# Kernel tuning notes

Measured on AMD Instinct MI355X. Metric: run time of the kernel, lower is better.

The kernel has to match this reference:

```python
import jax, jax.numpy as jnp
import numpy as np
from jax import lax

NPOINT = 1024
RADIUS = 0.2
NSAMPLE = 32


def fps(xyz, npoint):
    """Furthest point sampling on one cloud. xyz: (N,3) -> (npoint,) int32."""
    n = xyz.shape[0]
    init_d = jnp.full((n,), 1e10, xyz.dtype)

    def body(carry, _):
        dists, last_idx = carry
        last = xyz[last_idx]
        d = jnp.sum((xyz - last) ** 2, axis=-1)
        dists = jnp.minimum(dists, d)
        nxt = jnp.argmax(dists).astype(jnp.int32)
        return (dists, nxt), nxt

    (_, _), idxs = lax.scan(body, (init_d, jnp.int32(0)), None, length=npoint - 1)
    return jnp.concatenate([jnp.zeros((1,), jnp.int32), idxs])


def ball_query(xyz, new_xyz, radius, nsample):
    """First `nsample` points of xyz within `radius` of each center (pad with first hit).
    xyz: (N,3), new_xyz: (S,3) -> (S,nsample) int32."""
    n = xyz.shape[0]
    d2 = jnp.sum((new_xyz[:, None, :] - xyz[None, :, :]) ** 2, axis=-1)  # (S,N)
    cand = jnp.where(d2 < radius * radius, jnp.arange(n, dtype=jnp.int32)[None, :], n)
    idx = jnp.sort(cand, axis=1)[:, :nsample]                            # (S,K)
    first = jnp.where(idx[:, :1] == n, 0, idx[:, :1])
    return jnp.where(idx == n, first, idx)


def setup_inputs() -> dict:
    key = jax.random.key(0)
    ks = jax.random.split(key, 8)
    C_in = 64 + 3  # features + relative xyz
    W1 = jax.random.normal(ks[0], (64, C_in), jnp.float32) * (1.0 / np.sqrt(C_in))
    b1 = jnp.zeros((64,), jnp.float32)
    W2 = jax.random.normal(ks[1], (128, 64), jnp.float32) * (1.0 / np.sqrt(64))
    b2 = jnp.zeros((128,), jnp.float32)
    W3 = jax.random.normal(ks[2], (256, 128), jnp.float32) * (1.0 / np.sqrt(128))
    b3 = jnp.zeros((256,), jnp.float32)
    xyz = jax.random.uniform(ks[3], (8, 4096, 3), jnp.float32)
    features = jax.random.normal(ks[4], (8, 4096, 64), jnp.float32)
    return {"xyz": xyz, "features": features, "W1": W1, "b1": b1,
            "W2": W2, "b2": b2, "W3": W3, "b3": b3}


def reference(xyz, features, W1, b1, W2, b2, W3, b3):
    def per_batch(xyz_b, feat_b):
        fps_idx = fps(xyz_b, NPOINT)                      # (S,)
        new_xyz = xyz_b[fps_idx]                          # (S,3)
        idx = ball_query(xyz_b, new_xyz, RADIUS, NSAMPLE)  # (S,K)
        g_xyz = xyz_b[idx] - new_xyz[:, None, :]          # (S,K,3) relative coords
        g_feat = feat_b[idx]                              # (S,K,C)
        g = jnp.concatenate([g_xyz, g_feat], axis=-1)     # (S,K,3+C)
        x = jnp.transpose(g, (2, 0, 1))                   # (C',S,K)
        for W, b in ((W1, b1), (W2, b2), (W3, b3)):       # 1x1 conv + ReLU stack
            x = jax.nn.relu(jnp.einsum('oc,csk->osk', W, x) + b[:, None, None])
        return new_xyz, jnp.max(x, axis=-1), fps_idx      # max-pool over nsample

    new_xyz, new_features, sample_inds = jax.vmap(per_batch)(xyz, features)
    return new_xyz, new_features, sample_inds
```

## Files before the change

### kernel.cpp

```cpp
#include <hip/hip_runtime.h>
#include <stdint.h>

#define N_PTS 4096
#define S_PTS 1024
#define K_SAMP 32
#define NWORK 248
#define RSTRIDE 16

typedef __attribute__((ext_vector_type(8))) short bf16x8;
typedef __attribute__((ext_vector_type(4))) float f32x4;

#define GT1_S 104
#define GT2_S 72
#define GT3_S 136

__device__ __forceinline__ short f2b(float f){
  unsigned u = __float_as_uint(f);
  u = u + 0x7fffu + ((u >> 16) & 1u);
  return (short)(u >> 16);
}

#define DPP_QUAD_XOR1 0xB1
#define DPP_QUAD_XOR2 0x4E
#define DPP_ROW_HMIRR 0x141
#define DPP_ROW_MIRR  0x140
#define DPP_ROW_BC15  0x142
#define DPP_ROW_BC31  0x143

template<int CTRL>
__device__ __forceinline__ unsigned long long kstep(unsigned long long k){
  unsigned lo = (unsigned)k, hi = (unsigned)(k >> 32);
  unsigned lo2 = (unsigned)__builtin_amdgcn_update_dpp((int)lo, (int)lo, CTRL, 0xF, 0xF, false);
  unsigned hi2 = (unsigned)__builtin_amdgcn_update_dpp((int)hi, (int)hi, CTRL, 0xF, 0xF, false);
  unsigned long long ok = ((unsigned long long)hi2 << 32) | lo2;
  return ok > k ? ok : k;
}

__global__ void wconv_kernel(const float* __restrict__ W1,
                             const float* __restrict__ W2,
                             const float* __restrict__ W3,
                             short* __restrict__ ws_w,
                             int* __restrict__ ready){
  short* w1 = ws_w;
  short* w2 = ws_w + 64*96;
  short* w3 = ws_w + 64*96 + 128*64;
  int t = blockIdx.x * blockDim.x + threadIdx.x;
  int stride = gridDim.x * blockDim.x;
  for (int i = t; i < 8*S_PTS*RSTRIDE; i += stride) ready[i] = 0;
  for (int i = t; i < 64*96; i += stride){
    int m = i / 96, k = i - m*96;
    float v = 0.0f;
    if (k < 64)      v = W1[m*67 + 3 + k];
    else if (k < 67) v = W1[m*67 + (k - 64)];
    w1[i] = f2b(v);
  }
  for (int i = t; i < 128*64;  i += stride) w2[i] = f2b(W2[i]);
  for (int i = t; i < 256*128; i += stride) w3[i] = f2b(W3[i]);
}

template<int M, int KC, int KPAD, int GS_IN, int GS_OUT>
__device__ __forceinline__ void layer_mfma(const short* __restrict__ Wl,
                                           const short* gin, short* gout,
                                           const float* __restrict__ sbias_l,
                                           int w, int quad, int col){
  for (int m0 = w*16; m0 < M; m0 += 64){
    f32x4 acc0 = {0,0,0,0}, acc1 = {0,0,0,0};
#pragma unroll
    for (int kc = 0; kc < KC; ++kc){
      bf16x8 a  = *reinterpret_cast<const bf16x8*>(Wl + (size_t)(m0+col)*KPAD + kc*32 + quad*8);
      bf16x8 b0 = *reinterpret_cast<const bf16x8*>(gin + col*GS_IN + kc*32 + quad*8);
      bf16x8 b1 = *reinterpret_cast<const bf16x8*>(gin + (16+col)*GS_IN + kc*32 + quad*8);
      acc0 = __builtin_amdgcn_mfma_f32_16x16x32_bf16(a, b0, acc0, 0, 0, 0);
      acc1 = __builtin_amdgcn_mfma_f32_16x16x32_bf16(a, b1, acc1, 0, 0, 0);
    }
    int rbase = m0 + quad*4;
    unsigned long long P0 = 0ull, P1 = 0ull;
#pragma unroll
    for (int r = 0; r < 4; ++r){
      float bias = sbias_l[rbase + r];
      unsigned long long q0 = (unsigned short)f2b(fmaxf(acc0[r] + bias, 0.0f));
      unsigned long long q1 = (unsigned short)f2b(fmaxf(acc1[r] + bias, 0.0f));
      P0 |= q0 << (16*r);
      P1 |= q1 << (16*r);
    }
    *reinterpret_cast<unsigned long long*>(&gout[col*GS_OUT + rbase])      = P0;
    *reinterpret_cast<unsigned long long*>(&gout[(16+col)*GS_OUT + rbase]) = P1;
  }
}

__global__ __launch_bounds__(256) void fused_kernel(
    const float* __restrict__ xyz, const float* __restrict__ feat,
    const float* __restrict__ b1, const float* __restrict__ b2,
    const float* __restrict__ b3, const short* __restrict__ ws_w,
    float* __restrict__ out_newxyz, float* __restrict__ out_inds,
    int* __restrict__ ready, float* __restrict__ out_feat){

  __shared__ __align__(16) union ShU {
    struct { float4 c4[N_PTS]; unsigned long long slots[2][4]; } f;
    struct { short gT1[32*GT1_S]; short gT2[32*GT2_S]; short gT3[32*GT3_S];
             int sidx[K_SAMP]; float sbias[448]; int cidx; } m;
    char pad[82400];
  } sh;

  const int t = threadIdx.x;
  const int lane = t & 63;
  const int w = t >> 6;

  if (blockIdx.x < 8){
    const int b = blockIdx.x;
    const float* xb = xyz + (size_t)b * N_PTS * 3;

    float px[16], py[16], pz[16], dist[16];
#pragma unroll
    for (int j = 0; j < 16; ++j){
      int p = j * 256 + t;
      float x = xb[p*3+0], y = xb[p*3+1], z = xb[p*3+2];
      px[j] = x; py[j] = y; pz[j] = z; dist[j] = 1e10f;
      sh.f.c4[p] = make_float4(x, y, z, 0.0f);
    }
    __syncthreads();

    float lx, ly, lz;
    { float4 c0 = sh.f.c4[0]; lx = c0.x; ly = c0.y; lz = c0.z; }
    if (t == 0){
      out_inds[(size_t)b * S_PTS] = 0.0f;
      out_newxyz[(size_t)b*S_PTS*3 + 0] = lx;
      out_newxyz[(size_t)b*S_PTS*3 + 1] = ly;
      out_newxyz[(size_t)b*S_PTS*3 + 2] = lz;
      __hip_atomic_store(&ready[(size_t)b*S_PTS*RSTRIDE], 1,
                         __ATOMIC_RELAXED, __HIP_MEMORY_SCOPE_AGENT);
    }

    for (int it = 1; it < S_PTS; ++it){
      float bv = -1.0f; int bj = 0;
#pragma unroll
      for (int j = 0; j < 16; ++j){
        float dx = __fsub_rn(px[j], lx);
        float dy = __fsub_rn(py[j], ly);
        float dz = __fsub_rn(pz[j], lz);
        float d  = __fadd_rn(__fadd_rn(__fmul_rn(dx,dx), __fmul_rn(dy,dy)), __fmul_rn(dz,dz));
        float nd = fminf(dist[j], d);
        dist[j] = nd;
        bool gt = nd > bv;
        bv = gt ? nd : bv;
        bj = gt ? j  : bj;
      }
      int bi = bj * 256 + t;
      unsigned long long k = ((unsigned long long)__float_as_uint(bv) << 32)
                           | (unsigned)(~bi);

      k = kstep<DPP_QUAD_XOR1>(k);
      k = kstep<DPP_QUAD_XOR2>(k);
      k = kstep<DPP_ROW_HMIRR>(k);
      k = kstep<DPP_ROW_MIRR >(k);
      k = kstep<DPP_ROW_BC15 >(k);
      k = kstep<DPP_ROW_BC31 >(k);

      if (lane == 63) sh.f.slots[it & 1][w] = k;
      __syncthreads();

      unsigned long long sk = sh.f.slots[it & 1][lane & 3];
      sk = kstep<DPP_QUAD_XOR1>(sk);
      sk = kstep<DPP_QUAD_XOR2>(sk);
      int cur = (int)(~(unsigned)sk);

      float4 cc = sh.f.c4[cur];
      lx = cc.x; ly = cc.y; lz = cc.z;
      if (t == 0){
        out_inds[(size_t)b*S_PTS + it] = (float)cur;
        out_newxyz[((size_t)b*S_PTS + it)*3 + 0] = lx;
        out_newxyz[((size_t)b*S_PTS + it)*3 + 1] = ly;
        out_newxyz[((size_t)b*S_PTS + it)*3 + 2] = lz;
        __hip_atomic_store(&ready[((size_t)b*S_PTS + it)*RSTRIDE], cur + 1,
                           __ATOMIC_RELAXED, __HIP_MEMORY_SCOPE_AGENT);
      }
    }
    return;
  }

  const int wid = blockIdx.x - 8;
  const int quad = lane >> 4;
  const int col = lane & 15;
  const short* w1 = ws_w;
  const short* w2 = ws_w + 64*96;
  const short* w3 = ws_w + 64*96 + 128*64;

  for (int i = t; i < 448; i += 256)
    sh.m.sbias[i] = (i < 64) ? b1[i] : (i < 192) ? b2[i-64] : b3[i-192];
  for (int i = t; i < 32*GT1_S; i += 256) sh.m.gT1[i] = 0;

  for (int c = wid; c < 8*S_PTS; c += NWORK){
    const int b = c >> 10;
    const int s = c & (S_PTS - 1);

    if (t == 0){
      int v;
      while ((v = __hip_atomic_load(&ready[(size_t)c*RSTRIDE],
                                    __ATOMIC_RELAXED, __HIP_MEMORY_SCOPE_AGENT)) == 0)
        __builtin_amdgcn_s_sleep(4);
      sh.m.cidx = v - 1;
    }
    __syncthreads();
    const int cen = sh.m.cidx;
    const float* pc = xyz + ((size_t)b * N_PTS + cen) * 3;
    const float cx = pc[0], cy = pc[1], cz = pc[2];

    if (w == 0){
      const float* xb = xyz + (size_t)b * N_PTS * 3;
      const float R2 = 0.2f * 0.2f;
      int have = 0, first = -1;
      for (int chunk = 0; chunk < 64 && have < K_SAMP; ++chunk){
        int p = chunk * 64 + lane;
        float dx = __fsub_rn(xb[p*3+0], cx);
        float dy = __fsub_rn(xb[p*3+1], cy);
        float dz = __fsub_rn(xb[p*3+2], cz);
        float d2 = __fadd_rn(__fadd_rn(__fmul_rn(dx,dx), __fmul_rn(dy,dy)), __fmul_rn(dz,dz));
        bool hit = d2 < R2;
        unsigned long long mask = __ballot(hit);
        if (mask){
          if (first < 0) first = chunk*64 + (__ffsll(mask) - 1);
          int pre = __popcll(mask & ((1ull << lane) - 1ull));
          if (hit && (have + pre) < K_SAMP) sh.m.sidx[have + pre] = p;
          have += __popcll(mask);
          if (have > K_SAMP) have = K_SAMP;
        }
      }
      if (first < 0) first = 0;
      if (lane < K_SAMP - have) sh.m.sidx[have + lane] = first;
    }
    __syncthreads();

    {
      int p = t >> 3, q = t & 7;
      int src = sh.m.sidx[p];
      const float* fr = feat + ((size_t)b * N_PTS + src) * 64 + q*8;
      unsigned u[4];
#pragma unroll
      for (int jj = 0; jj < 4; ++jj){
        unsigned lo = (unsigned short)f2b(fr[2*jj]);
        unsigned hi = (unsigned short)f2b(fr[2*jj+1]);
        u[jj] = lo | (hi << 16);
      }
      uint4 v; v.x = u[0]; v.y = u[1]; v.z = u[2]; v.w = u[3];
      *reinterpret_cast<uint4*>(&sh.m.gT1[p*GT1_S + q*8]) = v;
    }
    if (t < 32){
      int src = sh.m.sidx[t];
      const float* pr = xyz + ((size_t)b * N_PTS + src) * 3;
      sh.m.gT1[t*GT1_S + 64] = f2b(__fsub_rn(pr[0], cx));
      sh.m.gT1[t*GT1_S + 65] = f2b(__fsub_rn(pr[1], cy));
      sh.m.gT1[t*GT1_S + 66] = f2b(__fsub_rn(pr[2], cz));
    }
    __syncthreads();

    layer_mfma<64, 3, 96, GT1_S, GT2_S>(w1, sh.m.gT1, sh.m.gT2, sh.m.sbias, w, quad, col);
    __syncthreads();
    layer_mfma<128, 2, 64, GT2_S, GT3_S>(w2, sh.m.gT2, sh.m.gT3, sh.m.sbias + 64, w, quad, col);
    __syncthreads();

    for (int m0 = w*16; m0 < 256; m0 += 64){
      f32x4 acc0 = {0,0,0,0}, acc1 = {0,0,0,0};
#pragma unroll
      for (int kc = 0; kc < 4; ++kc){
        bf16x8 a  = *reinterpret_cast<const bf16x8*>(w3 + (size_t)(m0+col)*128 + kc*32 + quad*8);
        bf16x8 b0 = *reinterpret_cast<const bf16x8*>(sh.m.gT3 + col*GT3_S + kc*32 + quad*8);
        bf16x8 b1 = *reinterpret_cast<const bf16x8*>(sh.m.gT3 + (16+col)*GT3_S + kc*32 + quad*8);
        acc0 = __builtin_amdgcn_mfma_f32_16x16x32_bf16(a, b0, acc0, 0, 0, 0);
        acc1 = __builtin_amdgcn_mfma_f32_16x16x32_bf16(a, b1, acc1, 0, 0, 0);
      }
      float vm[4];
#pragma unroll
      for (int r = 0; r < 4; ++r) vm[r] = fmaxf(acc0[r], acc1[r]);
#pragma unroll
      for (int off = 1; off < 16; off <<= 1){
#pragma unroll
        for (int r = 0; r < 4; ++r) vm[r] = fmaxf(vm[r], __shfl_xor(vm[r], off, 16));
      }
      if (col == 0){
#pragma unroll
        for (int r = 0; r < 4; ++r){
          int ch = m0 + quad*4 + r;
          out_feat[((size_t)b*256 + ch)*S_PTS + s] =
              fmaxf(vm[r] + sh.m.sbias[192 + ch], 0.0f);
        }
      }
    }
  }
}

extern "C" void kernel_launch(void* const* d_in, const int* in_sizes, int n_in,
                              void* d_out, int out_size, void* d_ws, size_t ws_size,
                              hipStream_t stream){
  const float* xyz  = (const float*)d_in[0];
  const float* feat = (const float*)d_in[1];
  const float* W1   = (const float*)d_in[2];
  const float* b1   = (const float*)d_in[3];
  const float* W2   = (const float*)d_in[4];
  const float* b2   = (const float*)d_in[5];
  const float* W3   = (const float*)d_in[6];
  const float* b3   = (const float*)d_in[7];

  float* out        = (float*)d_out;
  float* out_newxyz = out;
  float* out_feat   = out + 24576;
  float* out_inds   = out + 24576 + 2097152;

  char*  ws     = (char*)d_ws;
  short* ws_w   = (short*)ws;
  int*   ready  = (int*)(ws + 94208);

  wconv_kernel<<<32, 256, 0, stream>>>(W1, W2, W3, ws_w, ready);
  fused_kernel<<<8 + NWORK, 256, 0, stream>>>(xyz, feat, b1, b2, b3, ws_w,
                                              out_newxyz, out_inds, ready, out_feat);
}
```

Baseline: 992.3 us.

## Use dynamic work queue and keep consumers off FPS producer CUs

Replaces the static strided assignment of centroids to 248 consumer blocks with an atomic work counter fetched by 504 consumer blocks. Each FPS producer block publishes its CU/XCC id, and any consumer block landing on the same CU exits so it cannot steal cycles from the latency-critical FPS loop. The LDS padding that forced one block per CU is dropped, so several blocks can now share a CU. This adds atomic contention and a startup spin on producer registration, and relies on hardware-id registers to detect co-location.

```diff
diff --git a/kernel.cpp b/kernel.cpp
--- a/kernel.cpp
+++ b/kernel.cpp
@@ -4,7 +4,7 @@
 #define N_PTS 4096
 #define S_PTS 1024
 #define K_SAMP 32
-#define NWORK 248
+#define NCONS 504
 #define RSTRIDE 16
 
 typedef __attribute__((ext_vector_type(8))) short bf16x8;
@@ -18,6 +18,13 @@
   unsigned u = __float_as_uint(f);
   u = u + 0x7fffu + ((u >> 16) & 1u);
   return (short)(u >> 16);
+}
+
+__device__ __forceinline__ int cu_tag(){
+  unsigned hwid, xcc;
+  asm volatile("s_getreg_b32 %0, hwreg(HW_REG_HW_ID)" : "=s"(hwid));
+  asm volatile("s_getreg_b32 %0, hwreg(HW_REG_XCC_ID)" : "=s"(xcc));
+  return (int)(((hwid >> 8) & 0xFFu) | (xcc << 8)) + 1;
 }
 
 #define DPP_QUAD_XOR1 0xB1
@@ -40,12 +47,14 @@
                              const float* __restrict__ W2,
                              const float* __restrict__ W3,
                              short* __restrict__ ws_w,
-                             int* __restrict__ ready){
+                             int* __restrict__ ready,
+                             int* __restrict__ ctrl){
   short* w1 = ws_w;
   short* w2 = ws_w + 64*96;
   short* w3 = ws_w + 64*96 + 128*64;
   int t = blockIdx.x * blockDim.x + threadIdx.x;
   int stride = gridDim.x * blockDim.x;
+  if (t < 16) ctrl[t] = 0;
   for (int i = t; i < 8*S_PTS*RSTRIDE; i += stride) ready[i] = 0;
   for (int i = t; i < 64*96; i += stride){
     int m = i / 96, k = i - m*96;
@@ -93,13 +102,13 @@
     const float* __restrict__ b1, const float* __restrict__ b2,
     const float* __restrict__ b3, const short* __restrict__ ws_w,
     float* __restrict__ out_newxyz, float* __restrict__ out_inds,
-    int* __restrict__ ready, float* __restrict__ out_feat){
+    int* __restrict__ ready, int* __restrict__ ctrl,
+    float* __restrict__ out_feat){
 
   __shared__ __align__(16) union ShU {
     struct { float4 c4[N_PTS]; unsigned long long slots[2][4]; } f;
     struct { short gT1[32*GT1_S]; short gT2[32*GT2_S]; short gT3[32*GT3_S];
-             int sidx[K_SAMP]; float sbias[448]; int cidx; } m;
-    char pad[82400];
+             int sidx[K_SAMP]; float sbias[448]; int cidx; int qc; } m;
   } sh;
 
   const int t = threadIdx.x;
@@ -108,6 +117,9 @@
 
   if (blockIdx.x < 8){
     const int b = blockIdx.x;
+    if (t == 0)
+      __hip_atomic_store(&ctrl[b], cu_tag(),
+                         __ATOMIC_RELAXED, __HIP_MEMORY_SCOPE_AGENT);
     const float* xb = xyz + (size_t)b * N_PTS * 3;
 
     float px[16], py[16], pz[16], dist[16];
@@ -178,7 +190,18 @@
     return;
   }
 
-  const int wid = blockIdx.x - 8;
+  if (t == 0){
+    for (int i = 0; i < 8; ++i)
+      while (__hip_atomic_load(&ctrl[i], __ATOMIC_RELAXED, __HIP_MEMORY_SCOPE_AGENT) == 0)
+        __builtin_amdgcn_s_sleep(8);
+    int my = cu_tag(), on = 0;
+    for (int i = 0; i < 8; ++i)
+      on |= (__hip_atomic_load(&ctrl[i], __ATOMIC_RELAXED, __HIP_MEMORY_SCOPE_AGENT) == my);
+    sh.m.qc = on;
+  }
+  __syncthreads();
+  if (sh.m.qc) return;
+
   const int quad = lane >> 4;
   const int col = lane & 15;
   const short* w1 = ws_w;
@@ -189,18 +212,24 @@
     sh.m.sbias[i] = (i < 64) ? b1[i] : (i < 192) ? b2[i-64] : b3[i-192];
   for (int i = t; i < 32*GT1_S; i += 256) sh.m.gT1[i] = 0;
 
-  for (int c = wid; c < 8*S_PTS; c += NWORK){
+  for (;;){
+    if (t == 0){
+      int c = __hip_atomic_fetch_add(&ctrl[8], 1,
+                                     __ATOMIC_RELAXED, __HIP_MEMORY_SCOPE_AGENT);
+      sh.m.qc = c;
+      if (c < 8*S_PTS){
+        int v;
+        while ((v = __hip_atomic_load(&ready[(size_t)c*RSTRIDE],
+                                      __ATOMIC_RELAXED, __HIP_MEMORY_SCOPE_AGENT)) == 0)
+          __builtin_amdgcn_s_sleep(4);
+        sh.m.cidx = v - 1;
+      }
+    }
+    __syncthreads();
+    const int c = sh.m.qc;
+    if (c >= 8*S_PTS) break;
     const int b = c >> 10;
     const int s = c & (S_PTS - 1);
-
-    if (t == 0){
-      int v;
-      while ((v = __hip_atomic_load(&ready[(size_t)c*RSTRIDE],
-                                    __ATOMIC_RELAXED, __HIP_MEMORY_SCOPE_AGENT)) == 0)
-        __builtin_amdgcn_s_sleep(4);
-      sh.m.cidx = v - 1;
-    }
-    __syncthreads();
     const int cen = sh.m.cidx;
     const float* pc = xyz + ((size_t)b * N_PTS + cen) * 3;
     const float cx = pc[0], cy = pc[1], cz = pc[2];
@@ -308,8 +337,10 @@
   char*  ws     = (char*)d_ws;
   short* ws_w   = (short*)ws;
   int*   ready  = (int*)(ws + 94208);
-
-  wconv_kernel<<<32, 256, 0, stream>>>(W1, W2, W3, ws_w, ready);
-  fused_kernel<<<8 + NWORK, 256, 0, stream>>>(xyz, feat, b1, b2, b3, ws_w,
-                                              out_newxyz, out_inds, ready, out_feat);
-}
+  int*   ctrl   = (int*)(ws + 94208 + 524288);
+
+  wconv_kernel<<<32, 256, 0, stream>>>(W1, W2, W3, ws_w, ready, ctrl);
+  fused_kernel<<<8 + NCONS, 256, 0, stream>>>(xyz, feat, b1, b2, b3, ws_w,
+                                              out_newxyz, out_inds, ready, ctrl,
+                                              out_feat);
+}
```

After: 798.6 us. 1.24x faster.
